# Kernel tuning notes

Hardware: AMD Instinct MI355X
Metric: run time of the kernel (lower is better)

The kernel has to match this reference:

```python
import jax, jax.numpy as jnp
import numpy as np

NUM_HEADS = 16


def setup_inputs() -> dict:
    key = jax.random.key(0)
    ks = jax.random.split(key, 7)
    E = 1024
    s = 0.02
    return {
        "x": jax.random.normal(ks[0], (2, 2048, E), dtype=jnp.float32),
        "Wq": jax.random.normal(ks[1], (E, E), dtype=jnp.float32) * s,
        "bq": jax.random.normal(ks[2], (E,), dtype=jnp.float32) * s,
        "Wk": jax.random.normal(ks[3], (E, E), dtype=jnp.float32) * s,
        "bk": jax.random.normal(ks[4], (E,), dtype=jnp.float32) * s,
        "Wv": jax.random.normal(ks[5], (E, E), dtype=jnp.float32) * s,
        "bv": jax.random.normal(ks[6], (E,), dtype=jnp.float32) * s,
    }


def reference(x, Wq, bq, Wk, bk, Wv, bv):
    b, s, e = x.shape
    h = NUM_HEADS
    d = e // h  # head_dim = 64
    # nn.Linear: y = x @ W^T + b
    q = x @ Wq.T + bq
    k = x @ Wk.T + bk
    v = x @ Wv.T + bv
    # Faithful reshape chain from the source: (b,s,e)->(b,s,h,d)->(-1,s,d)
    # (raw reshape, NO transpose, matching the original buggy layout)
    q = q.reshape(b, s, h, d).reshape(-1, s, d)
    k = k.reshape(b, s, h, d).reshape(-1, s, d)
    v = v.reshape(b, s, h, d).reshape(-1, s, d)
    # Scaled scores; note the source returns qk @ v (softmax result discarded)
    scale = 1.0 / np.sqrt(d).astype(np.float32)
    qk = jnp.einsum('bqd,bkd->bqk', q, k) * scale  # [b*h, s, s]
    out = jnp.einsum('bqk,bkd->bqd', qk, v)        # [b*h, s, d]
    return out
```

## Files before the change

### kernel.cpp

```cpp
#include <hip/hip_runtime.h>
#include <hip/hip_bf16.h>


#define E_DIM 1024
#define N_ROWS 4096

typedef __attribute__((ext_vector_type(8))) short bf16x8;
typedef __attribute__((ext_vector_type(4))) float f32x4;

#define QB_U 0
#define KB_U 4194304
#define VB_U 8388608
#define XB_U 12582912
#define WB_U 16777216
#define P_F  9961472
#define TB_U 24117248

__device__ __forceinline__ unsigned short f2b(float f) {
    union { float f; unsigned int i; } c; c.f = f;
    unsigned int r = c.i + 0x7FFFu + ((c.i >> 16) & 1u);
    return (unsigned short)(r >> 16);
}

typedef __attribute__((address_space(1))) const void* gptr_t;
typedef __attribute__((address_space(3))) void* lptr_t;
__device__ __forceinline__ void gl_lds16(const void* g, void* l) {
    __builtin_amdgcn_global_load_lds((gptr_t)g, (lptr_t)l, 16, 0, 0);
}

__global__ __launch_bounds__(256) void cvt_bf16(
    const float* __restrict__ x,  const float* __restrict__ wq,
    const float* __restrict__ wk, const float* __restrict__ wv,
    unsigned short* __restrict__ dst0)
{
    const int seg = blockIdx.y;
    const float* __restrict__ src;
    unsigned short* __restrict__ dst;
    if (seg < 4) { src = x + (size_t)seg * 1048576; dst = dst0 + (size_t)seg * 1048576; }
    else {
        src = (seg == 4) ? wq : (seg == 5) ? wk : wv;
        dst = dst0 + 4194304 + (size_t)(seg - 4) * 1048576;
    }
    const int i = blockIdx.x * 256 + threadIdx.x;
    const float4 a = *(const float4*)(src + (size_t)i * 8);
    const float4 b = *(const float4*)(src + (size_t)i * 8 + 4);
    uint4 o;
    o.x = (unsigned)f2b(a.x) | ((unsigned)f2b(a.y) << 16);
    o.y = (unsigned)f2b(a.z) | ((unsigned)f2b(a.w) << 16);
    o.z = (unsigned)f2b(b.x) | ((unsigned)f2b(b.y) << 16);
    o.w = (unsigned)f2b(b.z) | ((unsigned)f2b(b.w) << 16);
    *(uint4*)(dst + (size_t)i * 8) = o;
}

__global__ __launch_bounds__(256, 3) void qkv_gemm_mfma(
    const unsigned short* __restrict__ Xb,
    const unsigned short* __restrict__ Wb,
    const float* __restrict__ bq, const float* __restrict__ bk,
    const float* __restrict__ bv,
    unsigned short* __restrict__ qkv)
{
    const int which = blockIdx.z;
    const unsigned short* __restrict__ W = Wb + (size_t)which * (1024 * 1024);
    const float* __restrict__ bias = (which == 0) ? bq : (which == 1) ? bk : bv;
    unsigned short* __restrict__ Y = qkv + (size_t)which * ((size_t)N_ROWS * E_DIM);

    __shared__ __align__(16) unsigned short Als[128 * 64];
    __shared__ __align__(16) unsigned short Bls[128 * 64];

    const int tid  = threadIdx.x;
    const int w    = tid >> 6;
    const int lane = tid & 63;
    const int m0 = blockIdx.x * 128;
    const int n0 = blockIdx.y * 128;
    const int wm = (w >> 1) * 64;
    const int wn = (w & 1) * 64;

    f32x4 acc[4][4];
    #pragma unroll
    for (int i = 0; i < 4; ++i)
        #pragma unroll
        for (int j = 0; j < 4; ++j)
            acc[i][j] = f32x4{0.f, 0.f, 0.f, 0.f};

    const int srow = lane >> 3;
    const int skc  = ((lane & 7) ^ (lane >> 3)) * 8;
    const int quad = lane >> 4;
    const int fm   = lane & 15;
    const int sw8  = fm & 7;

    for (int k0 = 0; k0 < E_DIM; k0 += 64) {
        #pragma unroll
        for (int c = 0; c < 4; ++c) {
            const int r = w * 32 + c * 8;
            gl_lds16((const void*)(Xb + (size_t)(m0 + r + srow) * E_DIM + k0 + skc),
                     (void*)((char*)Als + r * 128 + lane * 16));
            gl_lds16((const void*)(W + (size_t)(n0 + r + srow) * E_DIM + k0 + skc),
                     (void*)((char*)Bls + r * 128 + lane * 16));
        }
        __syncthreads();

        #pragma unroll
        for (int kk = 0; kk < 2; ++kk) {
            const int slot = ((kk * 4 + quad) ^ sw8) * 8;
            bf16x8 af[4], bf[4];
            #pragma unroll
            for (int t = 0; t < 4; ++t) {
                af[t] = *(const bf16x8*)(Als + (wm + t * 16 + fm) * 64 + slot);
                bf[t] = *(const bf16x8*)(Bls + (wn + t * 16 + fm) * 64 + slot);
            }
            #pragma unroll
            for (int rt = 0; rt < 4; ++rt)
                #pragma unroll
                for (int ct = 0; ct < 4; ++ct)
                    acc[rt][ct] = __builtin_amdgcn_mfma_f32_16x16x32_bf16(
                        af[rt], bf[ct], acc[rt][ct], 0, 0, 0);
        }
        __syncthreads();
    }

    float bcol[4];
    #pragma unroll
    for (int ct = 0; ct < 4; ++ct) bcol[ct] = bias[n0 + wn + ct * 16 + fm];

    const int rbase = (lane >> 4) * 4;
    #pragma unroll
    for (int rt = 0; rt < 4; ++rt) {
        #pragma unroll
        for (int ct = 0; ct < 4; ++ct) {
            #pragma unroll
            for (int r = 0; r < 4; ++r) {
                const int row = m0 + wm + rt * 16 + rbase + r;
                const int col = n0 + wn + ct * 16 + fm;
                Y[(size_t)row * E_DIM + col] = f2b(acc[rt][ct][r] + bcol[ct]);
            }
        }
    }
}

__device__ __forceinline__ int sw_idx(int row, int r) {
    return row * 64 + (((((r) >> 3) & 7) ^ (row & 7)) << 3) + (r & 7);
}

__global__ __launch_bounds__(256) void kT_mfma(
    const unsigned short* __restrict__ qkv, float* __restrict__ P)
{
    const size_t base = (size_t)blockIdx.x * (2048 * 64) + (size_t)blockIdx.y * (256 * 64);
    const unsigned short* __restrict__ Kb = qkv + KB_U + base;
    const unsigned short* __restrict__ Vb = qkv + VB_U + base;
    float* __restrict__ Pout = P + ((size_t)blockIdx.x * 8 + blockIdx.y) * 4096;

    __shared__ __align__(16) unsigned short Kt[64 * 64];
    __shared__ __align__(16) unsigned short Vt[64 * 64];

    const int tid  = threadIdx.x;
    const int w    = tid >> 6;
    const int lane = tid & 63;
    const int rl   = tid & 63;
    const int eo   = (tid >> 6) * 16;
    const int quad = lane >> 4;
    const int fm   = lane & 15;
    const int sw8  = fm & 7;

    f32x4 acc[4];
    #pragma unroll
    for (int nt = 0; nt < 4; ++nt) acc[nt] = f32x4{0.f, 0.f, 0.f, 0.f};

    for (int rb = 0; rb < 256; rb += 64) {
        union { uint4 u; unsigned short s[8]; } k0, k1, v0, v1;
        const size_t ga = (size_t)(rb + rl) * 64 + eo;
        k0.u = *(const uint4*)(Kb + ga);
        k1.u = *(const uint4*)(Kb + ga + 8);
        v0.u = *(const uint4*)(Vb + ga);
        v1.u = *(const uint4*)(Vb + ga + 8);
        __syncthreads();
        #pragma unroll
        for (int j = 0; j < 8; ++j) {
            Kt[sw_idx(eo + j, rl)]     = k0.s[j];
            Kt[sw_idx(eo + 8 + j, rl)] = k1.s[j];
            Vt[sw_idx(eo + j, rl)]     = v0.s[j];
            Vt[sw_idx(eo + 8 + j, rl)] = v1.s[j];
        }
        __syncthreads();
        #pragma unroll
        for (int kk = 0; kk < 2; ++kk) {
            const int slot = ((kk * 4 + quad) ^ sw8) << 3;
            const bf16x8 af = *(const bf16x8*)(Vt + (w * 16 + fm) * 64 + slot);
            #pragma unroll
            for (int nt = 0; nt < 4; ++nt) {
                const bf16x8 bf = *(const bf16x8*)(Kt + (nt * 16 + fm) * 64 + slot);
                acc[nt] = __builtin_amdgcn_mfma_f32_16x16x32_bf16(af, bf, acc[nt], 0, 0, 0);
            }
        }
    }

    const int rbase = (lane >> 4) * 4;
    #pragma unroll
    for (int nt = 0; nt < 4; ++nt)
        #pragma unroll
        for (int r = 0; r < 4; ++r)
            Pout[(size_t)(w * 16 + rbase + r) * 64 + nt * 16 + fm] = acc[nt][r];
}

__global__ __launch_bounds__(256) void reduce_T(
    const float* __restrict__ P, unsigned short* __restrict__ TB)
{
    const int idx = blockIdx.x * 256 + threadIdx.x;
    const int i   = idx >> 12;
    const int off = idx & 4095;
    const float* p = P + (size_t)i * 8 * 4096 + off;
    float s = 0.0f;
    #pragma unroll
    for (int c = 0; c < 8; ++c) s += p[(size_t)c * 4096];
    TB[(size_t)i * 4096 + off] = f2b(s);
}

__global__ __launch_bounds__(256, 2) void qT_mfma(
    const unsigned short* __restrict__ qkv,
    const unsigned short* __restrict__ TB,
    float* __restrict__ out)
{
    __shared__ __align__(16) unsigned short Als[128 * 64];
    __shared__ __align__(16) unsigned short Bls[64 * 64];

    const int bx   = blockIdx.x;
    const int r0   = bx * 128;
    const int i    = bx >> 4;
    const int tid  = threadIdx.x;
    const int w    = tid >> 6;
    const int lane = tid & 63;
    const int quad = lane >> 4;
    const int fm   = lane & 15;
    const int sw8  = fm & 7;

    const unsigned short* __restrict__ Qb = qkv + QB_U + (size_t)r0 * 64;
    const unsigned short* __restrict__ Tb = TB + (size_t)i * 4096;

    const int soff = (lane >> 3) * 64 + (((lane & 7) ^ (lane >> 3)) << 3);
    #pragma unroll
    for (int c = 0; c < 4; ++c)
        gl_lds16((const void*)(Qb + (w * 4 + c) * 512 + soff),
                 (void*)((char*)Als + (w * 4 + c) * 1024));
    #pragma unroll
    for (int c = 0; c < 2; ++c)
        gl_lds16((const void*)(Tb + (w * 2 + c) * 512 + soff),
                 (void*)((char*)Bls + (w * 2 + c) * 1024));
    __syncthreads();

    bf16x8 af[2][2], bf[4][2];
    #pragma unroll
    for (int mt = 0; mt < 2; ++mt)
        #pragma unroll
        for (int kk = 0; kk < 2; ++kk)
            af[mt][kk] = *(const bf16x8*)(Als + (w * 32 + mt * 16 + fm) * 64
                                          + (((kk * 4 + quad) ^ sw8) << 3));
    #pragma unroll
    for (int nt = 0; nt < 4; ++nt)
        #pragma unroll
        for (int kk = 0; kk < 2; ++kk)
            bf[nt][kk] = *(const bf16x8*)(Bls + (nt * 16 + fm) * 64
                                          + (((kk * 4 + quad) ^ sw8) << 3));

    f32x4 acc[2][4];
    #pragma unroll
    for (int mt = 0; mt < 2; ++mt)
        #pragma unroll
        for (int nt = 0; nt < 4; ++nt)
            acc[mt][nt] = f32x4{0.f, 0.f, 0.f, 0.f};

    #pragma unroll
    for (int kk = 0; kk < 2; ++kk)
        #pragma unroll
        for (int mt = 0; mt < 2; ++mt)
            #pragma unroll
            for (int nt = 0; nt < 4; ++nt)
                acc[mt][nt] = __builtin_amdgcn_mfma_f32_16x16x32_bf16(
                    af[mt][kk], bf[nt][kk], acc[mt][nt], 0, 0, 0);

    const int rbase = (lane >> 4) * 4;
    #pragma unroll
    for (int mt = 0; mt < 2; ++mt) {
        #pragma unroll
        for (int nt = 0; nt < 4; ++nt) {
            #pragma unroll
            for (int r = 0; r < 4; ++r) {
                const int row = r0 + w * 32 + mt * 16 + rbase + r;
                const int col = nt * 16 + fm;
                out[(size_t)row * 64 + col] = 0.125f * acc[mt][nt][r];
            }
        }
    }
}

extern "C" void kernel_launch(void* const* d_in, const int* in_sizes, int n_in,
                              void* d_out, int out_size, void* d_ws, size_t ws_size,
                              hipStream_t stream)
{
    const float* x  = (const float*)d_in[0];
    const float* Wq = (const float*)d_in[1];
    const float* bq = (const float*)d_in[2];
    const float* Wk = (const float*)d_in[3];
    const float* bk = (const float*)d_in[4];
    const float* Wv = (const float*)d_in[5];
    const float* bv = (const float*)d_in[6];
    float* wsf = (float*)d_ws;
    unsigned short* wsu = (unsigned short*)d_ws;
    float* out = (float*)d_out;

    dim3 gCvt(512, 7);
    cvt_bf16<<<gCvt, 256, 0, stream>>>(x, Wq, Wk, Wv, wsu + XB_U);

    dim3 gA(N_ROWS / 128, E_DIM / 128, 3);
    qkv_gemm_mfma<<<gA, 256, 0, stream>>>(wsu + XB_U, wsu + WB_U,
                                          bq, bk, bv, wsu + QB_U);

    dim3 gB(32, 8);
    kT_mfma<<<gB, 256, 0, stream>>>(wsu, wsf + P_F);

    reduce_T<<<512, 256, 0, stream>>>(wsf + P_F, wsu + TB_U);

    qT_mfma<<<512, 256, 0, stream>>>(wsu, wsu + TB_U, out);
}
```

Before: 129.0 us.

## Fuse Q projection, T reduction and Q·T product into one kernel

Splits the QKV GEMM so only K and V are projected up front. A new kernel computes the Q projection tile in registers, stores it swizzled into LDS, and reduces the partial K^T V sums into LDS inside the same block. It then multiplies Q by T directly to produce the output. This removes the Q round trip to global memory and two kernel launches. In exchange it uses more LDS per block and makes the Q GEMM run after the K/V chain instead of in parallel with it.

```diff
diff --git a/kernel.cpp b/kernel.cpp
--- a/kernel.cpp
+++ b/kernel.cpp
@@ -8,13 +8,11 @@
 typedef __attribute__((ext_vector_type(8))) short bf16x8;
 typedef __attribute__((ext_vector_type(4))) float f32x4;
 
-#define QB_U 0
 #define KB_U 4194304
 #define VB_U 8388608
 #define XB_U 12582912
 #define WB_U 16777216
 #define P_F  9961472
-#define TB_U 24117248
 
 __device__ __forceinline__ unsigned short f2b(float f) {
     union { float f; unsigned int i; } c; c.f = f;
@@ -22,10 +20,23 @@
     return (unsigned short)(r >> 16);
 }
 
+__device__ __forceinline__ uint4 pack8(const f32x4 a, const f32x4 b) {
+    uint4 o;
+    o.x = (unsigned)f2b(a[0]) | ((unsigned)f2b(a[1]) << 16);
+    o.y = (unsigned)f2b(a[2]) | ((unsigned)f2b(a[3]) << 16);
+    o.z = (unsigned)f2b(b[0]) | ((unsigned)f2b(b[1]) << 16);
+    o.w = (unsigned)f2b(b[2]) | ((unsigned)f2b(b[3]) << 16);
+    return o;
+}
+
 typedef __attribute__((address_space(1))) const void* gptr_t;
 typedef __attribute__((address_space(3))) void* lptr_t;
 __device__ __forceinline__ void gl_lds16(const void* g, void* l) {
     __builtin_amdgcn_global_load_lds((gptr_t)g, (lptr_t)l, 16, 0, 0);
+}
+
+__device__ __forceinline__ int sw_idx(int row, int r) {
+    return row * 64 + (((((r) >> 3) & 7) ^ (row & 7)) << 3) + (r & 7);
 }
 
 __global__ __launch_bounds__(256) void cvt_bf16(
@@ -52,16 +63,15 @@
     *(uint4*)(dst + (size_t)i * 8) = o;
 }
 
-__global__ __launch_bounds__(256, 3) void qkv_gemm_mfma(
+__global__ __launch_bounds__(256, 3) void kv_gemm_mfma(
     const unsigned short* __restrict__ Xb,
     const unsigned short* __restrict__ Wb,
-    const float* __restrict__ bq, const float* __restrict__ bk,
-    const float* __restrict__ bv,
+    const float* __restrict__ bk, const float* __restrict__ bv,
     unsigned short* __restrict__ qkv)
 {
-    const int which = blockIdx.z;
+    const int which = blockIdx.z + 1;
     const unsigned short* __restrict__ W = Wb + (size_t)which * (1024 * 1024);
-    const float* __restrict__ bias = (which == 0) ? bq : (which == 1) ? bk : bv;
+    const float* __restrict__ bias = (which == 1) ? bk : bv;
     unsigned short* __restrict__ Y = qkv + (size_t)which * ((size_t)N_ROWS * E_DIM);
 
     __shared__ __align__(16) unsigned short Als[128 * 64];
@@ -135,10 +145,6 @@
             }
         }
     }
-}
-
-__device__ __forceinline__ int sw_idx(int row, int r) {
-    return row * 64 + (((((r) >> 3) & 7) ^ (row & 7)) << 3) + (r & 7);
 }
 
 __global__ __launch_bounds__(256) void kT_mfma(
@@ -201,91 +207,145 @@
             Pout[(size_t)(w * 16 + rbase + r) * 64 + nt * 16 + fm] = acc[nt][r];
 }
 
-__global__ __launch_bounds__(256) void reduce_T(
-    const float* __restrict__ P, unsigned short* __restrict__ TB)
-{
-    const int idx = blockIdx.x * 256 + threadIdx.x;
-    const int i   = idx >> 12;
-    const int off = idx & 4095;
-    const float* p = P + (size_t)i * 8 * 4096 + off;
-    float s = 0.0f;
-    #pragma unroll
-    for (int c = 0; c < 8; ++c) s += p[(size_t)c * 4096];
-    TB[(size_t)i * 4096 + off] = f2b(s);
-}
-
-__global__ __launch_bounds__(256, 2) void qT_mfma(
-    const unsigned short* __restrict__ qkv,
-    const unsigned short* __restrict__ TB,
+__global__ __launch_bounds__(256, 2) void q_gemm_out(
+    const unsigned short* __restrict__ Xb,
+    const unsigned short* __restrict__ Wb,
+    const float* __restrict__ bq,
+    const float* __restrict__ P,
     float* __restrict__ out)
 {
-    __shared__ __align__(16) unsigned short Als[128 * 64];
-    __shared__ __align__(16) unsigned short Bls[64 * 64];
-
-    const int bx   = blockIdx.x;
-    const int r0   = bx * 128;
-    const int i    = bx >> 4;
+    __shared__ __align__(16) unsigned short S[20480];
+    unsigned short* Als = S;
+    unsigned short* Bls = S + 8192;
+    unsigned short* Tls = S + 16384;
+
     const int tid  = threadIdx.x;
     const int w    = tid >> 6;
     const int lane = tid & 63;
+    const int m0 = blockIdx.x * 128;
+    const int n0 = blockIdx.y * 128;
+    const int wm = (w >> 1) * 64;
+    const int wn = (w & 1) * 64;
     const int quad = lane >> 4;
     const int fm   = lane & 15;
     const int sw8  = fm & 7;
-
-    const unsigned short* __restrict__ Qb = qkv + QB_U + (size_t)r0 * 64;
-    const unsigned short* __restrict__ Tb = TB + (size_t)i * 4096;
-
-    const int soff = (lane >> 3) * 64 + (((lane & 7) ^ (lane >> 3)) << 3);
-    #pragma unroll
-    for (int c = 0; c < 4; ++c)
-        gl_lds16((const void*)(Qb + (w * 4 + c) * 512 + soff),
-                 (void*)((char*)Als + (w * 4 + c) * 1024));
-    #pragma unroll
-    for (int c = 0; c < 2; ++c)
-        gl_lds16((const void*)(Tb + (w * 2 + c) * 512 + soff),
-                 (void*)((char*)Bls + (w * 2 + c) * 1024));
+    const int srow = lane >> 3;
+    const int skc  = ((lane & 7) ^ (lane >> 3)) * 8;
+
+    {
+        const int d  = tid >> 2;
+        const int e0 = (tid & 3) << 4;
+        const float* p = P + (size_t)blockIdx.x * 32768 + (size_t)d * 64 + e0;
+        f32x4 s0{0.f,0.f,0.f,0.f}, s1{0.f,0.f,0.f,0.f};
+        f32x4 s2{0.f,0.f,0.f,0.f}, s3{0.f,0.f,0.f,0.f};
+        #pragma unroll
+        for (int c = 0; c < 8; ++c) {
+            s0 += *(const f32x4*)(p + (size_t)c * 4096);
+            s1 += *(const f32x4*)(p + (size_t)c * 4096 + 4);
+            s2 += *(const f32x4*)(p + (size_t)c * 4096 + 8);
+            s3 += *(const f32x4*)(p + (size_t)c * 4096 + 12);
+        }
+        const int c0 = e0 >> 3;
+        *(uint4*)(Tls + d * 64 + ((c0 ^ (d & 7)) << 3))       = pack8(s0, s1);
+        *(uint4*)(Tls + d * 64 + (((c0 + 1) ^ (d & 7)) << 3)) = pack8(s2, s3);
+    }
+
+    f32x4 acc[4][4];
+    #pragma unroll
+    for (int i = 0; i < 4; ++i)
+        #pragma unroll
+        for (int j = 0; j < 4; ++j)
+            acc[i][j] = f32x4{0.f, 0.f, 0.f, 0.f};
+
+    for (int k0 = 0; k0 < E_DIM; k0 += 64) {
+        #pragma unroll
+        for (int c = 0; c < 4; ++c) {
+            const int r = w * 32 + c * 8;
+            gl_lds16((const void*)(Xb + (size_t)(m0 + r + srow) * E_DIM + k0 + skc),
+                     (void*)((char*)Als + r * 128 + lane * 16));
+            gl_lds16((const void*)(Wb + (size_t)(n0 + r + srow) * E_DIM + k0 + skc),
+                     (void*)((char*)Bls + r * 128 + lane * 16));
+        }
+        __syncthreads();
+
+        #pragma unroll
+        for (int kk = 0; kk < 2; ++kk) {
+            const int slot = ((kk * 4 + quad) ^ sw8) * 8;
+            bf16x8 af[4], bf[4];
+            #pragma unroll
+            for (int t = 0; t < 4; ++t) {
+                af[t] = *(const bf16x8*)(Als + (wm + t * 16 + fm) * 64 + slot);
+                bf[t] = *(const bf16x8*)(Bls + (wn + t * 16 + fm) * 64 + slot);
+            }
+            #pragma unroll
+            for (int rt = 0; rt < 4; ++rt)
+                #pragma unroll
+                for (int ct = 0; ct < 4; ++ct)
+                    acc[rt][ct] = __builtin_amdgcn_mfma_f32_16x16x32_bf16(
+                        af[rt], bf[ct], acc[rt][ct], 0, 0, 0);
+        }
+        __syncthreads();
+    }
+
+    float bcol[4];
+    #pragma unroll
+    for (int ct = 0; ct < 4; ++ct) bcol[ct] = bq[n0 + wn + ct * 16 + fm];
+
+    const int rbase = (lane >> 4) * 4;
+    #pragma unroll
+    for (int rt = 0; rt < 4; ++rt) {
+        #pragma unroll
+        for (int ct = 0; ct < 4; ++ct) {
+            const int cl = wn + ct * 16 + fm;
+            const int hb = (cl >> 6) << 13;
+            const int e  = cl & 63;
+            #pragma unroll
+            for (int r = 0; r < 4; ++r) {
+                const int row = wm + rt * 16 + rbase + r;
+                S[hb + sw_idx(row, e)] = f2b(acc[rt][ct][r] + bcol[ct]);
+            }
+        }
+    }
     __syncthreads();
 
-    bf16x8 af[2][2], bf[4][2];
-    #pragma unroll
-    for (int mt = 0; mt < 2; ++mt)
-        #pragma unroll
-        for (int kk = 0; kk < 2; ++kk)
-            af[mt][kk] = *(const bf16x8*)(Als + (w * 32 + mt * 16 + fm) * 64
-                                          + (((kk * 4 + quad) ^ sw8) << 3));
-    #pragma unroll
-    for (int nt = 0; nt < 4; ++nt)
-        #pragma unroll
-        for (int kk = 0; kk < 2; ++kk)
-            bf[nt][kk] = *(const bf16x8*)(Bls + (nt * 16 + fm) * 64
-                                          + (((kk * 4 + quad) ^ sw8) << 3));
-
-    f32x4 acc[2][4];
-    #pragma unroll
-    for (int mt = 0; mt < 2; ++mt)
-        #pragma unroll
-        for (int nt = 0; nt < 4; ++nt)
-            acc[mt][nt] = f32x4{0.f, 0.f, 0.f, 0.f};
-
-    #pragma unroll
-    for (int kk = 0; kk < 2; ++kk)
-        #pragma unroll
-        for (int mt = 0; mt < 2; ++mt)
+    const int hl = w & 1;
+    const int rh = w >> 1;
+    const unsigned short* Qs = S + hl * 8192;
+
+    f32x4 acc2[4][4];
+    #pragma unroll
+    for (int i = 0; i < 4; ++i)
+        #pragma unroll
+        for (int j = 0; j < 4; ++j)
+            acc2[i][j] = f32x4{0.f, 0.f, 0.f, 0.f};
+
+    #pragma unroll
+    for (int kk = 0; kk < 2; ++kk) {
+        const int slot = ((kk * 4 + quad) ^ sw8) << 3;
+        bf16x8 a2[4], b2[4];
+        #pragma unroll
+        for (int t = 0; t < 4; ++t) {
+            a2[t] = *(const bf16x8*)(Qs + (rh * 64 + t * 16 + fm) * 64 + slot);
+            b2[t] = *(const bf16x8*)(Tls + (t * 16 + fm) * 64 + slot);
+        }
+        #pragma unroll
+        for (int mt = 0; mt < 4; ++mt)
             #pragma unroll
             for (int nt = 0; nt < 4; ++nt)
-                acc[mt][nt] = __builtin_amdgcn_mfma_f32_16x16x32_bf16(
-                    af[mt][kk], bf[nt][kk], acc[mt][nt], 0, 0, 0);
-
-    const int rbase = (lane >> 4) * 4;
-    #pragma unroll
-    for (int mt = 0; mt < 2; ++mt) {
+                acc2[mt][nt] = __builtin_amdgcn_mfma_f32_16x16x32_bf16(
+                    a2[mt], b2[nt], acc2[mt][nt], 0, 0, 0);
+    }
+
+    const int h = blockIdx.y * 2 + hl;
+    #pragma unroll
+    for (int mt = 0; mt < 4; ++mt) {
         #pragma unroll
         for (int nt = 0; nt < 4; ++nt) {
             #pragma unroll
             for (int r = 0; r < 4; ++r) {
-                const int row = r0 + w * 32 + mt * 16 + rbase + r;
-                const int col = nt * 16 + fm;
-                out[(size_t)row * 64 + col] = 0.125f * acc[mt][nt][r];
+                const int grow = m0 + rh * 64 + mt * 16 + rbase + r;
+                const size_t fr = (size_t)grow * 16 + h;
+                out[fr * 64 + nt * 16 + fm] = 0.125f * acc2[mt][nt][r];
             }
         }
     }
@@ -309,14 +369,14 @@
     dim3 gCvt(512, 7);
     cvt_bf16<<<gCvt, 256, 0, stream>>>(x, Wq, Wk, Wv, wsu + XB_U);
 
-    dim3 gA(N_ROWS / 128, E_DIM / 128, 3);
-    qkv_gemm_mfma<<<gA, 256, 0, stream>>>(wsu + XB_U, wsu + WB_U,
-                                          bq, bk, bv, wsu + QB_U);
+    dim3 gKV(N_ROWS / 128, E_DIM / 128, 2);
+    kv_gemm_mfma<<<gKV, 256, 0, stream>>>(wsu + XB_U, wsu + WB_U,
+                                          bk, bv, wsu);
 
     dim3 gB(32, 8);
     kT_mfma<<<gB, 256, 0, stream>>>(wsu, wsf + P_F);
 
-    reduce_T<<<512, 256, 0, stream>>>(wsf + P_F, wsu + TB_U);
-
-    qT_mfma<<<512, 256, 0, stream>>>(wsu, wsu + TB_U, out);
-}
+    dim3 gQ(32, 8);
+    q_gemm_out<<<gQ, 256, 0, stream>>>(wsu + XB_U, wsu + WB_U,
+                                       bq, wsf + P_F, out);
+}
```

Result: slower. 137.9 us (+6.9%).

## Fuse GEMM, K^T V, reduction and Q-projection stages into one persistent kernel

Applied to the files above, without the earlier changes.

Merges the four kernels after conversion into a single 768-block kernel whose stages are separated by a software grid barrier built on an atomic counter. The counter is reset inside the conversion kernel. The goal is to remove the launch gaps and tail idle time between the small dependent kernels. In exchange it adds grid-wide spin barriers, which need all 768 blocks to be resident at once (3 per CU is assumed), or the kernel can deadlock. Blocks also sit idle during the smaller stages.

```diff
diff --git a/kernel.cpp b/kernel.cpp
--- a/kernel.cpp
+++ b/kernel.cpp
@@ -14,7 +14,10 @@
 #define XB_U 12582912
 #define WB_U 16777216
 #define P_F  9961472
+#define BAR_F 11010048
 #define TB_U 24117248
+
+#define NBLK 768u
 
 __device__ __forceinline__ unsigned short f2b(float f) {
     union { float f; unsigned int i; } c; c.f = f;
@@ -28,11 +31,28 @@
     __builtin_amdgcn_global_load_lds((gptr_t)g, (lptr_t)l, 16, 0, 0);
 }
 
+__device__ __forceinline__ int sw_idx(int row, int r) {
+    return row * 64 + (((((r) >> 3) & 7) ^ (row & 7)) << 3) + (r & 7);
+}
+
+__device__ __forceinline__ void gsync(unsigned* bar, unsigned target) {
+    __syncthreads();
+    if (threadIdx.x == 0) {
+        __threadfence();
+        __hip_atomic_fetch_add(bar, 1u, __ATOMIC_RELEASE, __HIP_MEMORY_SCOPE_AGENT);
+        while (__hip_atomic_load(bar, __ATOMIC_ACQUIRE, __HIP_MEMORY_SCOPE_AGENT) < target)
+            __builtin_amdgcn_s_sleep(2);
+        __threadfence();
+    }
+    __syncthreads();
+}
+
 __global__ __launch_bounds__(256) void cvt_bf16(
     const float* __restrict__ x,  const float* __restrict__ wq,
     const float* __restrict__ wk, const float* __restrict__ wv,
-    unsigned short* __restrict__ dst0)
+    unsigned short* __restrict__ dst0, unsigned* __restrict__ bar)
 {
+    if (blockIdx.x == 0 && blockIdx.y == 0 && threadIdx.x == 0) *bar = 0u;
     const int seg = blockIdx.y;
     const float* __restrict__ src;
     unsigned short* __restrict__ dst;
@@ -52,240 +72,222 @@
     *(uint4*)(dst + (size_t)i * 8) = o;
 }
 
-__global__ __launch_bounds__(256, 3) void qkv_gemm_mfma(
+__global__ __launch_bounds__(256, 3) void mega(
     const unsigned short* __restrict__ Xb,
     const unsigned short* __restrict__ Wb,
     const float* __restrict__ bq, const float* __restrict__ bk,
     const float* __restrict__ bv,
-    unsigned short* __restrict__ qkv)
+    unsigned short* __restrict__ qkv,
+    float* __restrict__ P,
+    unsigned short* __restrict__ TB,
+    float* __restrict__ out,
+    unsigned* __restrict__ bar)
 {
-    const int which = blockIdx.z;
-    const unsigned short* __restrict__ W = Wb + (size_t)which * (1024 * 1024);
-    const float* __restrict__ bias = (which == 0) ? bq : (which == 1) ? bk : bv;
-    unsigned short* __restrict__ Y = qkv + (size_t)which * ((size_t)N_ROWS * E_DIM);
-
-    __shared__ __align__(16) unsigned short Als[128 * 64];
-    __shared__ __align__(16) unsigned short Bls[128 * 64];
-
-    const int tid  = threadIdx.x;
-    const int w    = tid >> 6;
-    const int lane = tid & 63;
-    const int m0 = blockIdx.x * 128;
-    const int n0 = blockIdx.y * 128;
-    const int wm = (w >> 1) * 64;
-    const int wn = (w & 1) * 64;
-
-    f32x4 acc[4][4];
-    #pragma unroll
-    for (int i = 0; i < 4; ++i)
-        #pragma unroll
-        for (int j = 0; j < 4; ++j)
-            acc[i][j] = f32x4{0.f, 0.f, 0.f, 0.f};
-
-    const int srow = lane >> 3;
-    const int skc  = ((lane & 7) ^ (lane >> 3)) * 8;
-    const int quad = lane >> 4;
-    const int fm   = lane & 15;
-    const int sw8  = fm & 7;
-
-    for (int k0 = 0; k0 < E_DIM; k0 += 64) {
-        #pragma unroll
-        for (int c = 0; c < 4; ++c) {
-            const int r = w * 32 + c * 8;
-            gl_lds16((const void*)(Xb + (size_t)(m0 + r + srow) * E_DIM + k0 + skc),
-                     (void*)((char*)Als + r * 128 + lane * 16));
-            gl_lds16((const void*)(W + (size_t)(n0 + r + srow) * E_DIM + k0 + skc),
-                     (void*)((char*)Bls + r * 128 + lane * 16));
-        }
-        __syncthreads();
-
-        #pragma unroll
-        for (int kk = 0; kk < 2; ++kk) {
-            const int slot = ((kk * 4 + quad) ^ sw8) * 8;
-            bf16x8 af[4], bf[4];
-            #pragma unroll
-            for (int t = 0; t < 4; ++t) {
-                af[t] = *(const bf16x8*)(Als + (wm + t * 16 + fm) * 64 + slot);
-                bf[t] = *(const bf16x8*)(Bls + (wn + t * 16 + fm) * 64 + slot);
-            }
-            #pragma unroll
-            for (int rt = 0; rt < 4; ++rt)
-                #pragma unroll
-                for (int ct = 0; ct < 4; ++ct)
-                    acc[rt][ct] = __builtin_amdgcn_mfma_f32_16x16x32_bf16(
-                        af[rt], bf[ct], acc[rt][ct], 0, 0, 0);
-        }
-        __syncthreads();
-    }
-
-    float bcol[4];
-    #pragma unroll
-    for (int ct = 0; ct < 4; ++ct) bcol[ct] = bias[n0 + wn + ct * 16 + fm];
-
-    const int rbase = (lane >> 4) * 4;
-    #pragma unroll
-    for (int rt = 0; rt < 4; ++rt) {
-        #pragma unroll
-        for (int ct = 0; ct < 4; ++ct) {
-            #pragma unroll
-            for (int r = 0; r < 4; ++r) {
-                const int row = m0 + wm + rt * 16 + rbase + r;
-                const int col = n0 + wn + ct * 16 + fm;
-                Y[(size_t)row * E_DIM + col] = f2b(acc[rt][ct][r] + bcol[ct]);
-            }
-        }
-    }
-}
-
-__device__ __forceinline__ int sw_idx(int row, int r) {
-    return row * 64 + (((((r) >> 3) & 7) ^ (row & 7)) << 3) + (r & 7);
-}
-
-__global__ __launch_bounds__(256) void kT_mfma(
-    const unsigned short* __restrict__ qkv, float* __restrict__ P)
-{
-    const size_t base = (size_t)blockIdx.x * (2048 * 64) + (size_t)blockIdx.y * (256 * 64);
-    const unsigned short* __restrict__ Kb = qkv + KB_U + base;
-    const unsigned short* __restrict__ Vb = qkv + VB_U + base;
-    float* __restrict__ Pout = P + ((size_t)blockIdx.x * 8 + blockIdx.y) * 4096;
-
-    __shared__ __align__(16) unsigned short Kt[64 * 64];
-    __shared__ __align__(16) unsigned short Vt[64 * 64];
-
-    const int tid  = threadIdx.x;
-    const int w    = tid >> 6;
-    const int lane = tid & 63;
-    const int rl   = tid & 63;
-    const int eo   = (tid >> 6) * 16;
-    const int quad = lane >> 4;
-    const int fm   = lane & 15;
-    const int sw8  = fm & 7;
-
-    f32x4 acc[4];
-    #pragma unroll
-    for (int nt = 0; nt < 4; ++nt) acc[nt] = f32x4{0.f, 0.f, 0.f, 0.f};
-
-    for (int rb = 0; rb < 256; rb += 64) {
-        union { uint4 u; unsigned short s[8]; } k0, k1, v0, v1;
-        const size_t ga = (size_t)(rb + rl) * 64 + eo;
-        k0.u = *(const uint4*)(Kb + ga);
-        k1.u = *(const uint4*)(Kb + ga + 8);
-        v0.u = *(const uint4*)(Vb + ga);
-        v1.u = *(const uint4*)(Vb + ga + 8);
-        __syncthreads();
-        #pragma unroll
-        for (int j = 0; j < 8; ++j) {
-            Kt[sw_idx(eo + j, rl)]     = k0.s[j];
-            Kt[sw_idx(eo + 8 + j, rl)] = k1.s[j];
-            Vt[sw_idx(eo + j, rl)]     = v0.s[j];
-            Vt[sw_idx(eo + 8 + j, rl)] = v1.s[j];
-        }
-        __syncthreads();
-        #pragma unroll
-        for (int kk = 0; kk < 2; ++kk) {
-            const int slot = ((kk * 4 + quad) ^ sw8) << 3;
-            const bf16x8 af = *(const bf16x8*)(Vt + (w * 16 + fm) * 64 + slot);
-            #pragma unroll
-            for (int nt = 0; nt < 4; ++nt) {
-                const bf16x8 bf = *(const bf16x8*)(Kt + (nt * 16 + fm) * 64 + slot);
-                acc[nt] = __builtin_amdgcn_mfma_f32_16x16x32_bf16(af, bf, acc[nt], 0, 0, 0);
-            }
-        }
-    }
-
-    const int rbase = (lane >> 4) * 4;
-    #pragma unroll
-    for (int nt = 0; nt < 4; ++nt)
-        #pragma unroll
-        for (int r = 0; r < 4; ++r)
-            Pout[(size_t)(w * 16 + rbase + r) * 64 + nt * 16 + fm] = acc[nt][r];
-}
-
-__global__ __launch_bounds__(256) void reduce_T(
-    const float* __restrict__ P, unsigned short* __restrict__ TB)
-{
-    const int idx = blockIdx.x * 256 + threadIdx.x;
-    const int i   = idx >> 12;
-    const int off = idx & 4095;
-    const float* p = P + (size_t)i * 8 * 4096 + off;
-    float s = 0.0f;
-    #pragma unroll
-    for (int c = 0; c < 8; ++c) s += p[(size_t)c * 4096];
-    TB[(size_t)i * 4096 + off] = f2b(s);
-}
-
-__global__ __launch_bounds__(256, 2) void qT_mfma(
-    const unsigned short* __restrict__ qkv,
-    const unsigned short* __restrict__ TB,
-    float* __restrict__ out)
-{
-    __shared__ __align__(16) unsigned short Als[128 * 64];
-    __shared__ __align__(16) unsigned short Bls[64 * 64];
-
-    const int bx   = blockIdx.x;
-    const int r0   = bx * 128;
-    const int i    = bx >> 4;
+    __shared__ __align__(16) unsigned short S[16384];
+
+    const int b    = blockIdx.x;
     const int tid  = threadIdx.x;
     const int w    = tid >> 6;
     const int lane = tid & 63;
     const int quad = lane >> 4;
     const int fm   = lane & 15;
     const int sw8  = fm & 7;
-
-    const unsigned short* __restrict__ Qb = qkv + QB_U + (size_t)r0 * 64;
-    const unsigned short* __restrict__ Tb = TB + (size_t)i * 4096;
-
-    const int soff = (lane >> 3) * 64 + (((lane & 7) ^ (lane >> 3)) << 3);
-    #pragma unroll
-    for (int c = 0; c < 4; ++c)
-        gl_lds16((const void*)(Qb + (w * 4 + c) * 512 + soff),
-                 (void*)((char*)Als + (w * 4 + c) * 1024));
-    #pragma unroll
-    for (int c = 0; c < 2; ++c)
-        gl_lds16((const void*)(Tb + (w * 2 + c) * 512 + soff),
-                 (void*)((char*)Bls + (w * 2 + c) * 1024));
-    __syncthreads();
-
-    bf16x8 af[2][2], bf[4][2];
-    #pragma unroll
-    for (int mt = 0; mt < 2; ++mt)
+    const int rbase = quad * 4;
+
+    {
+        const int which = b >> 8;
+        const unsigned short* __restrict__ W = Wb + (size_t)which * (1024 * 1024);
+        const float* __restrict__ bias = (which == 0) ? bq : (which == 1) ? bk : bv;
+        unsigned short* __restrict__ Y = qkv + (size_t)which * ((size_t)N_ROWS * E_DIM);
+        const int m0 = (b & 31) * 128;
+        const int n0 = ((b >> 5) & 7) * 128;
+        const int wm = (w >> 1) * 64;
+        const int wn = (w & 1) * 64;
+        unsigned short* Als = S;
+        unsigned short* Bls = S + 8192;
+
+        f32x4 acc[4][4];
+        #pragma unroll
+        for (int i = 0; i < 4; ++i)
+            #pragma unroll
+            for (int j = 0; j < 4; ++j)
+                acc[i][j] = f32x4{0.f, 0.f, 0.f, 0.f};
+
+        const int srow = lane >> 3;
+        const int skc  = ((lane & 7) ^ (lane >> 3)) * 8;
+
+        for (int k0 = 0; k0 < E_DIM; k0 += 64) {
+            #pragma unroll
+            for (int c = 0; c < 4; ++c) {
+                const int r = w * 32 + c * 8;
+                gl_lds16((const void*)(Xb + (size_t)(m0 + r + srow) * E_DIM + k0 + skc),
+                         (void*)((char*)Als + r * 128 + lane * 16));
+                gl_lds16((const void*)(W + (size_t)(n0 + r + srow) * E_DIM + k0 + skc),
+                         (void*)((char*)Bls + r * 128 + lane * 16));
+            }
+            __syncthreads();
+
+            #pragma unroll
+            for (int kk = 0; kk < 2; ++kk) {
+                const int slot = ((kk * 4 + quad) ^ sw8) * 8;
+                bf16x8 af[4], bf[4];
+                #pragma unroll
+                for (int t = 0; t < 4; ++t) {
+                    af[t] = *(const bf16x8*)(Als + (wm + t * 16 + fm) * 64 + slot);
+                    bf[t] = *(const bf16x8*)(Bls + (wn + t * 16 + fm) * 64 + slot);
+                }
+                #pragma unroll
+                for (int rt = 0; rt < 4; ++rt)
+                    #pragma unroll
+                    for (int ct = 0; ct < 4; ++ct)
+                        acc[rt][ct] = __builtin_amdgcn_mfma_f32_16x16x32_bf16(
+                            af[rt], bf[ct], acc[rt][ct], 0, 0, 0);
+            }
+            __syncthreads();
+        }
+
+        float bcol[4];
+        #pragma unroll
+        for (int ct = 0; ct < 4; ++ct) bcol[ct] = bias[n0 + wn + ct * 16 + fm];
+
+        #pragma unroll
+        for (int rt = 0; rt < 4; ++rt) {
+            #pragma unroll
+            for (int ct = 0; ct < 4; ++ct) {
+                #pragma unroll
+                for (int r = 0; r < 4; ++r) {
+                    const int row = m0 + wm + rt * 16 + rbase + r;
+                    const int col = n0 + wn + ct * 16 + fm;
+                    Y[(size_t)row * E_DIM + col] = f2b(acc[rt][ct][r] + bcol[ct]);
+                }
+            }
+        }
+    }
+
+    gsync(bar, NBLK);
+
+    if (b < 256) {
+        unsigned short* Kt = S;
+        unsigned short* Vt = S + 4096;
+        const size_t base = (size_t)(b >> 3) * (2048 * 64) + (size_t)(b & 7) * (256 * 64);
+        const unsigned short* __restrict__ Kb = qkv + KB_U + base;
+        const unsigned short* __restrict__ Vb = qkv + VB_U + base;
+        float* __restrict__ Pout = P + (size_t)b * 4096;
+        const int eo = w * 16;
+
+        f32x4 acc[4];
+        #pragma unroll
+        for (int nt = 0; nt < 4; ++nt) acc[nt] = f32x4{0.f, 0.f, 0.f, 0.f};
+
+        for (int rb = 0; rb < 256; rb += 64) {
+            union { uint4 u; unsigned short s[8]; } k0, k1, v0, v1;
+            const size_t ga = (size_t)(rb + lane) * 64 + eo;
+            k0.u = *(const uint4*)(Kb + ga);
+            k1.u = *(const uint4*)(Kb + ga + 8);
+            v0.u = *(const uint4*)(Vb + ga);
+            v1.u = *(const uint4*)(Vb + ga + 8);
+            __syncthreads();
+            #pragma unroll
+            for (int j = 0; j < 8; ++j) {
+                Kt[sw_idx(eo + j, lane)]     = k0.s[j];
+                Kt[sw_idx(eo + 8 + j, lane)] = k1.s[j];
+                Vt[sw_idx(eo + j, lane)]     = v0.s[j];
+                Vt[sw_idx(eo + 8 + j, lane)] = v1.s[j];
+            }
+            __syncthreads();
+            #pragma unroll
+            for (int kk = 0; kk < 2; ++kk) {
+                const int slot = ((kk * 4 + quad) ^ sw8) << 3;
+                const bf16x8 af = *(const bf16x8*)(Vt + (w * 16 + fm) * 64 + slot);
+                #pragma unroll
+                for (int nt = 0; nt < 4; ++nt) {
+                    const bf16x8 bf = *(const bf16x8*)(Kt + (nt * 16 + fm) * 64 + slot);
+                    acc[nt] = __builtin_amdgcn_mfma_f32_16x16x32_bf16(af, bf, acc[nt], 0, 0, 0);
+                }
+            }
+        }
+
+        #pragma unroll
+        for (int nt = 0; nt < 4; ++nt)
+            #pragma unroll
+            for (int r = 0; r < 4; ++r)
+                Pout[(size_t)(w * 16 + rbase + r) * 64 + nt * 16 + fm] = acc[nt][r];
+    }
+
+    gsync(bar, 2u * NBLK);
+
+    if (b < 512) {
+        const int idx = b * 256 + tid;
+        const int i   = idx >> 12;
+        const int off = idx & 4095;
+        const float* p = P + (size_t)i * 8 * 4096 + off;
+        float s = 0.0f;
+        #pragma unroll
+        for (int c = 0; c < 8; ++c) s += p[(size_t)c * 4096];
+        TB[(size_t)i * 4096 + off] = f2b(s);
+    }
+
+    gsync(bar, 3u * NBLK);
+
+    if (b < 512) {
+        unsigned short* Als = S;
+        unsigned short* Bls = S + 8192;
+        const int r0 = b * 128;
+        const int i  = b >> 4;
+        const unsigned short* __restrict__ Qb = qkv + QB_U + (size_t)r0 * 64;
+        const unsigned short* __restrict__ Tb = TB + (size_t)i * 4096;
+
+        const int soff = (lane >> 3) * 64 + (((lane & 7) ^ (lane >> 3)) << 3);
+        #pragma unroll
+        for (int c = 0; c < 4; ++c)
+            gl_lds16((const void*)(Qb + (w * 4 + c) * 512 + soff),
+                     (void*)((char*)Als + (w * 4 + c) * 1024));
+        #pragma unroll
+        for (int c = 0; c < 2; ++c)
+            gl_lds16((const void*)(Tb + (w * 2 + c) * 512 + soff),
+                     (void*)((char*)Bls + (w * 2 + c) * 1024));
+        __syncthreads();
+
+        bf16x8 af[2][2], bf[4][2];
+        #pragma unroll
+        for (int mt = 0; mt < 2; ++mt)
+            #pragma unroll
+            for (int kk = 0; kk < 2; ++kk)
+                af[mt][kk] = *(const bf16x8*)(Als + (w * 32 + mt * 16 + fm) * 64
+                                              + (((kk * 4 + quad) ^ sw8) << 3));
+        #pragma unroll
+        for (int nt = 0; nt < 4; ++nt)
+            #pragma unroll
+            for (int kk = 0; kk < 2; ++kk)
+                bf[nt][kk] = *(const bf16x8*)(Bls + (nt * 16 + fm) * 64
+                                              + (((kk * 4 + quad) ^ sw8) << 3));
+
+        f32x4 acc[2][4];
+        #pragma unroll
+        for (int mt = 0; mt < 2; ++mt)
+            #pragma unroll
+            for (int nt = 0; nt < 4; ++nt)
+                acc[mt][nt] = f32x4{0.f, 0.f, 0.f, 0.f};
+
         #pragma unroll
         for (int kk = 0; kk < 2; ++kk)
-            af[mt][kk] = *(const bf16x8*)(Als + (w * 32 + mt * 16 + fm) * 64
-                                          + (((kk * 4 + quad) ^ sw8) << 3));
-    #pragma unroll
-    for (int nt = 0; nt < 4; ++nt)
-        #pragma unroll
-        for (int kk = 0; kk < 2; ++kk)
-            bf[nt][kk] = *(const bf16x8*)(Bls + (nt * 16 + fm) * 64
-                                          + (((kk * 4 + quad) ^ sw8) << 3));
-
-    f32x4 acc[2][4];
-    #pragma unroll
-    for (int mt = 0; mt < 2; ++mt)
-        #pragma unroll
-        for (int nt = 0; nt < 4; ++nt)
-            acc[mt][nt] = f32x4{0.f, 0.f, 0.f, 0.f};
-
-    #pragma unroll
-    for (int kk = 0; kk < 2; ++kk)
-        #pragma unroll
-        for (int mt = 0; mt < 2; ++mt)
-            #pragma unroll
-            for (int nt = 0; nt < 4; ++nt)
-                acc[mt][nt] = __builtin_amdgcn_mfma_f32_16x16x32_bf16(
-                    af[mt][kk], bf[nt][kk], acc[mt][nt], 0, 0, 0);
-
-    const int rbase = (lane >> 4) * 4;
-    #pragma unroll
-    for (int mt = 0; mt < 2; ++mt) {
-        #pragma unroll
-        for (int nt = 0; nt < 4; ++nt) {
-            #pragma unroll
-            for (int r = 0; r < 4; ++r) {
-                const int row = r0 + w * 32 + mt * 16 + rbase + r;
-                const int col = nt * 16 + fm;
-                out[(size_t)row * 64 + col] = 0.125f * acc[mt][nt][r];
+            #pragma unroll
+            for (int mt = 0; mt < 2; ++mt)
+                #pragma unroll
+                for (int nt = 0; nt < 4; ++nt)
+                    acc[mt][nt] = __builtin_amdgcn_mfma_f32_16x16x32_bf16(
+                        af[mt][kk], bf[nt][kk], acc[mt][nt], 0, 0, 0);
+
+        #pragma unroll
+        for (int mt = 0; mt < 2; ++mt) {
+            #pragma unroll
+            for (int nt = 0; nt < 4; ++nt) {
+                #pragma unroll
+                for (int r = 0; r < 4; ++r) {
+                    const int row = r0 + w * 32 + mt * 16 + rbase + r;
+                    const int col = nt * 16 + fm;
+                    out[(size_t)row * 64 + col] = 0.125f * acc[mt][nt][r];
+                }
             }
         }
     }
@@ -305,18 +307,13 @@
     float* wsf = (float*)d_ws;
     unsigned short* wsu = (unsigned short*)d_ws;
     float* out = (float*)d_out;
+    unsigned* bar = (unsigned*)(wsf + BAR_F);
 
     dim3 gCvt(512, 7);
-    cvt_bf16<<<gCvt, 256, 0, stream>>>(x, Wq, Wk, Wv, wsu + XB_U);
-
-    dim3 gA(N_ROWS / 128, E_DIM / 128, 3);
-    qkv_gemm_mfma<<<gA, 256, 0, stream>>>(wsu + XB_U, wsu + WB_U,
-                                          bq, bk, bv, wsu + QB_U);
-
-    dim3 gB(32, 8);
-    kT_mfma<<<gB, 256, 0, stream>>>(wsu, wsf + P_F);
-
-    reduce_T<<<512, 256, 0, stream>>>(wsf + P_F, wsu + TB_U);
-
-    qT_mfma<<<512, 256, 0, stream>>>(wsu, wsu + TB_U, out);
-}
+    cvt_bf16<<<gCvt, 256, 0, stream>>>(x, Wq, Wk, Wv, wsu + XB_U, bar);
+
+    mega<<<dim3(NBLK), 256, 0, stream>>>(wsu + XB_U, wsu + WB_U,
+                                         bq, bk, bv,
+                                         wsu, wsf + P_F, wsu + TB_U,
+                                         out, bar);
+}
```

Measured after the change: 469.5 us. 264% more time.

## Fuse partial-sum reduction into final GEMM and double K^T V split

Applied to the files above, without the earlier changes.

Removes the separate reduce_T kernel. Each block of the final Q·T GEMM now sums the fp32 partial K^T V tiles itself, converts them to bf16 and writes them swizzled into LDS. The K^T V stage is split into 16 chunks per head instead of 8 for more parallelism. Block indices are remapped so blocks sharing a head run together. The cost is that every block redundantly re-reads 16 partial tiles for its head, which adds global/L2 traffic.

```diff
diff --git a/kernel.cpp b/kernel.cpp
--- a/kernel.cpp
+++ b/kernel.cpp
@@ -14,7 +14,6 @@
 #define XB_U 12582912
 #define WB_U 16777216
 #define P_F  9961472
-#define TB_U 24117248
 
 __device__ __forceinline__ unsigned short f2b(float f) {
     union { float f; unsigned int i; } c; c.f = f;
@@ -22,10 +21,23 @@
     return (unsigned short)(r >> 16);
 }
 
+__device__ __forceinline__ uint4 pack8(const f32x4 a, const f32x4 b) {
+    uint4 o;
+    o.x = (unsigned)f2b(a[0]) | ((unsigned)f2b(a[1]) << 16);
+    o.y = (unsigned)f2b(a[2]) | ((unsigned)f2b(a[3]) << 16);
+    o.z = (unsigned)f2b(b[0]) | ((unsigned)f2b(b[1]) << 16);
+    o.w = (unsigned)f2b(b[2]) | ((unsigned)f2b(b[3]) << 16);
+    return o;
+}
+
 typedef __attribute__((address_space(1))) const void* gptr_t;
 typedef __attribute__((address_space(3))) void* lptr_t;
 __device__ __forceinline__ void gl_lds16(const void* g, void* l) {
     __builtin_amdgcn_global_load_lds((gptr_t)g, (lptr_t)l, 16, 0, 0);
+}
+
+__device__ __forceinline__ int sw_idx(int row, int r) {
+    return row * 64 + (((((r) >> 3) & 7) ^ (row & 7)) << 3) + (r & 7);
 }
 
 __global__ __launch_bounds__(256) void cvt_bf16(
@@ -137,17 +149,13 @@
     }
 }
 
-__device__ __forceinline__ int sw_idx(int row, int r) {
-    return row * 64 + (((((r) >> 3) & 7) ^ (row & 7)) << 3) + (r & 7);
-}
-
 __global__ __launch_bounds__(256) void kT_mfma(
     const unsigned short* __restrict__ qkv, float* __restrict__ P)
 {
-    const size_t base = (size_t)blockIdx.x * (2048 * 64) + (size_t)blockIdx.y * (256 * 64);
+    const size_t base = (size_t)blockIdx.x * (2048 * 64) + (size_t)blockIdx.y * (128 * 64);
     const unsigned short* __restrict__ Kb = qkv + KB_U + base;
     const unsigned short* __restrict__ Vb = qkv + VB_U + base;
-    float* __restrict__ Pout = P + ((size_t)blockIdx.x * 8 + blockIdx.y) * 4096;
+    float* __restrict__ Pout = P + ((size_t)blockIdx.x * 16 + blockIdx.y) * 4096;
 
     __shared__ __align__(16) unsigned short Kt[64 * 64];
     __shared__ __align__(16) unsigned short Vt[64 * 64];
@@ -155,8 +163,7 @@
     const int tid  = threadIdx.x;
     const int w    = tid >> 6;
     const int lane = tid & 63;
-    const int rl   = tid & 63;
-    const int eo   = (tid >> 6) * 16;
+    const int eo   = w * 16;
     const int quad = lane >> 4;
     const int fm   = lane & 15;
     const int sw8  = fm & 7;
@@ -165,9 +172,9 @@
     #pragma unroll
     for (int nt = 0; nt < 4; ++nt) acc[nt] = f32x4{0.f, 0.f, 0.f, 0.f};
 
-    for (int rb = 0; rb < 256; rb += 64) {
+    for (int rb = 0; rb < 128; rb += 64) {
         union { uint4 u; unsigned short s[8]; } k0, k1, v0, v1;
-        const size_t ga = (size_t)(rb + rl) * 64 + eo;
+        const size_t ga = (size_t)(rb + lane) * 64 + eo;
         k0.u = *(const uint4*)(Kb + ga);
         k1.u = *(const uint4*)(Kb + ga + 8);
         v0.u = *(const uint4*)(Vb + ga);
@@ -175,10 +182,10 @@
         __syncthreads();
         #pragma unroll
         for (int j = 0; j < 8; ++j) {
-            Kt[sw_idx(eo + j, rl)]     = k0.s[j];
-            Kt[sw_idx(eo + 8 + j, rl)] = k1.s[j];
-            Vt[sw_idx(eo + j, rl)]     = v0.s[j];
-            Vt[sw_idx(eo + 8 + j, rl)] = v1.s[j];
+            Kt[sw_idx(eo + j, lane)]     = k0.s[j];
+            Kt[sw_idx(eo + 8 + j, lane)] = k1.s[j];
+            Vt[sw_idx(eo + j, lane)]     = v0.s[j];
+            Vt[sw_idx(eo + 8 + j, lane)] = v1.s[j];
         }
         __syncthreads();
         #pragma unroll
@@ -201,30 +208,18 @@
             Pout[(size_t)(w * 16 + rbase + r) * 64 + nt * 16 + fm] = acc[nt][r];
 }
 
-__global__ __launch_bounds__(256) void reduce_T(
-    const float* __restrict__ P, unsigned short* __restrict__ TB)
-{
-    const int idx = blockIdx.x * 256 + threadIdx.x;
-    const int i   = idx >> 12;
-    const int off = idx & 4095;
-    const float* p = P + (size_t)i * 8 * 4096 + off;
-    float s = 0.0f;
-    #pragma unroll
-    for (int c = 0; c < 8; ++c) s += p[(size_t)c * 4096];
-    TB[(size_t)i * 4096 + off] = f2b(s);
-}
-
-__global__ __launch_bounds__(256, 2) void qT_mfma(
+__global__ __launch_bounds__(256, 2) void qT_fused(
     const unsigned short* __restrict__ qkv,
-    const unsigned short* __restrict__ TB,
+    const float* __restrict__ P,
     float* __restrict__ out)
 {
     __shared__ __align__(16) unsigned short Als[128 * 64];
-    __shared__ __align__(16) unsigned short Bls[64 * 64];
-
-    const int bx   = blockIdx.x;
-    const int r0   = bx * 128;
-    const int i    = bx >> 4;
+    __shared__ __align__(16) unsigned short Tls[64 * 64];
+
+    const int b    = blockIdx.x;
+    const int i    = (b & 7) + ((b >> 3) & 3) * 8;
+    const int sub  = b >> 5;
+    const int r0   = (i * 16 + sub) * 128;
     const int tid  = threadIdx.x;
     const int w    = tid >> 6;
     const int lane = tid & 63;
@@ -233,17 +228,30 @@
     const int sw8  = fm & 7;
 
     const unsigned short* __restrict__ Qb = qkv + QB_U + (size_t)r0 * 64;
-    const unsigned short* __restrict__ Tb = TB + (size_t)i * 4096;
 
     const int soff = (lane >> 3) * 64 + (((lane & 7) ^ (lane >> 3)) << 3);
     #pragma unroll
     for (int c = 0; c < 4; ++c)
         gl_lds16((const void*)(Qb + (w * 4 + c) * 512 + soff),
                  (void*)((char*)Als + (w * 4 + c) * 1024));
-    #pragma unroll
-    for (int c = 0; c < 2; ++c)
-        gl_lds16((const void*)(Tb + (w * 2 + c) * 512 + soff),
-                 (void*)((char*)Bls + (w * 2 + c) * 1024));
+
+    {
+        const int d  = tid >> 2;
+        const int e0 = (tid & 3) << 4;
+        const float* p = P + (size_t)i * 65536 + (size_t)d * 64 + e0;
+        f32x4 s0{0.f,0.f,0.f,0.f}, s1{0.f,0.f,0.f,0.f};
+        f32x4 s2{0.f,0.f,0.f,0.f}, s3{0.f,0.f,0.f,0.f};
+        #pragma unroll
+        for (int c = 0; c < 16; ++c) {
+            s0 += *(const f32x4*)(p + (size_t)c * 4096);
+            s1 += *(const f32x4*)(p + (size_t)c * 4096 + 4);
+            s2 += *(const f32x4*)(p + (size_t)c * 4096 + 8);
+            s3 += *(const f32x4*)(p + (size_t)c * 4096 + 12);
+        }
+        const int c0 = e0 >> 3;
+        *(uint4*)(Tls + d * 64 + ((c0 ^ (d & 7)) << 3))       = pack8(s0, s1);
+        *(uint4*)(Tls + d * 64 + (((c0 + 1) ^ (d & 7)) << 3)) = pack8(s2, s3);
+    }
     __syncthreads();
 
     bf16x8 af[2][2], bf[4][2];
@@ -257,7 +265,7 @@
     for (int nt = 0; nt < 4; ++nt)
         #pragma unroll
         for (int kk = 0; kk < 2; ++kk)
-            bf[nt][kk] = *(const bf16x8*)(Bls + (nt * 16 + fm) * 64
+            bf[nt][kk] = *(const bf16x8*)(Tls + (nt * 16 + fm) * 64
                                           + (((kk * 4 + quad) ^ sw8) << 3));
 
     f32x4 acc[2][4];
@@ -311,12 +319,10 @@
 
     dim3 gA(N_ROWS / 128, E_DIM / 128, 3);
     qkv_gemm_mfma<<<gA, 256, 0, stream>>>(wsu + XB_U, wsu + WB_U,
-                                          bq, bk, bv, wsu + QB_U);
-
-    dim3 gB(32, 8);
+                                          bq, bk, bv, wsu);
+
+    dim3 gB(32, 16);
     kT_mfma<<<gB, 256, 0, stream>>>(wsu, wsf + P_F);
 
-    reduce_T<<<512, 256, 0, stream>>>(wsf + P_F, wsu + TB_U);
-
-    qT_mfma<<<512, 256, 0, stream>>>(wsu, wsu + TB_U, out);
-}
+    qT_fused<<<512, 256, 0, stream>>>(wsu, wsf + P_F, out);
+}
```

New measurement: 132.3 us. 1.03x slower.
